# Optimization experiments

Hardware: AMD Instinct MI355X
Metric: run time of the kernel (lower is better)

## Reference

```python
import jax, jax.numpy as jnp
import numpy as np

B, LQ, LK, H = 4, 256, 512, 256

def setup_inputs() -> dict:
    key = jax.random.key(0)
    ks = jax.random.split(key, 9)
    return {
        "query": jax.random.normal(ks[0], (B, LQ, H), dtype=jnp.float32),
        "key": jax.random.normal(ks[1], (B, LK, H), dtype=jnp.float32),
        "value": jax.random.normal(ks[2], (B, LK, H), dtype=jnp.float32),
        "mask": jax.random.randint(ks[3], (B, LK), 0, 2, dtype=jnp.int32),
        "Wq": jax.random.normal(ks[4], (H, H), dtype=jnp.float32) / np.sqrt(H),
        "bq": jnp.zeros((H,), dtype=jnp.float32),
        "Wk": jax.random.normal(ks[5], (H, H), dtype=jnp.float32) / np.sqrt(H),
        "bk": jnp.zeros((H,), dtype=jnp.float32),
        "v": jax.random.normal(ks[6], (H,), dtype=jnp.float32) / np.sqrt(H),
        "bv": jnp.zeros((), dtype=jnp.float32),
    }

def reference(query, key, value, mask, Wq, bq, Wk, bk, v, bv):
    # Linear projections: y = x @ W^T + b (torch nn.Linear convention)
    q = query @ Wq.T + bq            # [B, Lq, H]
    k = key @ Wk.T + bk              # [B, Lk, H]
    # Broadcast add -> tanh -> project to scalar with v
    s = jnp.tanh(q[:, :, None, :] + k[:, None, :, :])   # [B, Lq, Lk, H]
    scores = jnp.einsum('bqkh,h->bqk', s, v) + bv        # [B, Lq, Lk]
    scores = jnp.where(mask[:, None, :] == 0, -jnp.inf, scores)
    attn_weights = jax.nn.softmax(scores, axis=-1)       # [B, Lq, Lk]
    attn_output = jnp.einsum('bqk,bkh->bqh', attn_weights, value)
    return (attn_output, attn_weights)
```

## Files before the change

kernel.cpp:

```cpp
#include <hip/hip_runtime.h>
#include <math.h>

#define NB  4
#define NLQ 256
#define NLK 512
#define NH  256

#define SCALE_2LOG2E 2.885390081777927f
#define LOG2E        1.4426950408889634f

__global__ __launch_bounds__(256) void setup_kernel(
    const float* __restrict__ Wq, const float* __restrict__ Wk,
    const int* __restrict__ mask,
    float* __restrict__ Wtq, float* __restrict__ Wtk,
    int* __restrict__ act, int* __restrict__ nact)
{
    const int blk = blockIdx.x;
    const int t   = threadIdx.x;

    if (blk < 32) {
        __shared__ float ts[64][65];
        const int m    = blk >> 4;
        const int tile = blk & 15;
        const int h0 = (tile >> 2) * 64;
        const int c0 = (tile & 3) * 64;
        const float* W  = m ? Wk  : Wq;
        float*       Wt = m ? Wtk : Wtq;
        const int lr = t >> 4, lc = t & 15;
        #pragma unroll
        for (int i = 0; i < 4; ++i) {
            const int r = lr + 16 * i;
            const float4 d = *(const float4*)(W + (size_t)(h0 + r) * NH + c0 + lc * 4);
            ts[r][lc * 4 + 0] = d.x;
            ts[r][lc * 4 + 1] = d.y;
            ts[r][lc * 4 + 2] = d.z;
            ts[r][lc * 4 + 3] = d.w;
        }
        __syncthreads();
        #pragma unroll
        for (int i = 0; i < 4; ++i) {
            const int c = lr + 16 * i;
            float4 d;
            d.x = ts[lc * 4 + 0][c];
            d.y = ts[lc * 4 + 1][c];
            d.z = ts[lc * 4 + 2][c];
            d.w = ts[lc * 4 + 3][c];
            *(float4*)(Wt + (size_t)(c0 + c) * NH + h0 + lc * 4) = d;
        }
    } else if (blk < 32 + NB) {
        const int b = blk - 32;
        __shared__ int wcnt[8], wpre[9];
        const int lane = t & 63, wave = t >> 6;
        const int k1 = t, k2 = t + 256;
        const int m1 = mask[b * NLK + k1];
        const int m2 = mask[b * NLK + k2];
        const unsigned long long below = (1ULL << lane) - 1ULL;
        const unsigned long long bal1 = __ballot(m1 != 0);
        const unsigned long long bal2 = __ballot(m2 != 0);
        const int r1 = __popcll(bal1 & below);
        const int r2 = __popcll(bal2 & below);
        if (lane == 0) { wcnt[wave] = __popcll(bal1); wcnt[4 + wave] = __popcll(bal2); }
        __syncthreads();
        if (t == 0) {
            int s = 0;
            #pragma unroll
            for (int w = 0; w < 8; ++w) { wpre[w] = s; s += wcnt[w]; }
            wpre[8] = s;
        }
        __syncthreads();
        const int na = wpre[8];
        if (m1) act[b * NLK + wpre[wave]     + r1] = k1;
        if (m2) act[b * NLK + wpre[4 + wave] + r2] = k2;
        if (k1 >= na) act[b * NLK + k1] = 0;
        if (k2 >= na) act[b * NLK + k2] = 0;
        if (t == 0) nact[b] = na;
    }
}

__global__ __launch_bounds__(256) void prep_kernel(
    const float* __restrict__ query, const float* __restrict__ key,
    const float* __restrict__ Wtq, const float* __restrict__ bq,
    const float* __restrict__ Wtk, const float* __restrict__ bk,
    const int* __restrict__ act, const int* __restrict__ nact,
    float* __restrict__ qp, float* __restrict__ kp_ct)
{
    const int blk  = blockIdx.x;
    const int t    = threadIdx.x;
    const int wave = t >> 6;
    const int lane = t & 63;

    __shared__ float  xs[4][NH];
    __shared__ float4 ps[4][4][64];
    __shared__ int    ridx[4];

    const float *Wt, *bias;
    int b = 0, j0 = 0, r0 = 0, na = 0;
    const bool isq = (blk < NB * NLQ / 4);

    if (isq) {
        r0 = blk * 4;
        ((float4*)&xs[0][0])[t] = ((const float4*)(query + (size_t)r0 * NH))[t];
        Wt = Wtq; bias = bq;
    } else {
        b  = (blk - 256) >> 7;
        j0 = ((blk - 256) & 127) * 4;
        na = nact[b];
        if (j0 >= na) return;
        if (t < 4) ridx[t] = act[b * NLK + ((j0 + t < na) ? (j0 + t) : j0)];
        __syncthreads();
        const int r = t >> 6, c4 = t & 63;
        ((float4*)xs[r])[c4] =
            ((const float4*)(key + ((size_t)b * NLK + ridx[r]) * NH))[c4];
        Wt = Wtk; bias = bk;
    }
    __syncthreads();

    float4 acc[4];
    #pragma unroll
    for (int r = 0; r < 4; ++r) acc[r] = (float4){0.f, 0.f, 0.f, 0.f};

    const int cbase = wave * 64;
    #pragma unroll 4
    for (int cc = 0; cc < 64; ++cc) {
        const int c = cbase + cc;
        const float4 w = *(const float4*)(Wt + (size_t)c * NH + lane * 4);
        #pragma unroll
        for (int r = 0; r < 4; ++r) {
            const float xv = xs[r][c];
            acc[r].x = fmaf(xv, w.x, acc[r].x);
            acc[r].y = fmaf(xv, w.y, acc[r].y);
            acc[r].z = fmaf(xv, w.z, acc[r].z);
            acc[r].w = fmaf(xv, w.w, acc[r].w);
        }
    }
    #pragma unroll
    for (int r = 0; r < 4; ++r) ps[wave][r][lane] = acc[r];
    __syncthreads();

    const int r = wave, l = lane;
    const float4 p0 = ps[0][r][l], p1 = ps[1][r][l];
    const float4 p2 = ps[2][r][l], p3 = ps[3][r][l];
    const float4 bb = *(const float4*)(bias + l * 4);
    float4 o;
    o.x = (p0.x + p1.x + p2.x + p3.x + bb.x) * SCALE_2LOG2E;
    o.y = (p0.y + p1.y + p2.y + p3.y + bb.y) * SCALE_2LOG2E;
    o.z = (p0.z + p1.z + p2.z + p3.z + bb.z) * SCALE_2LOG2E;
    o.w = (p0.w + p1.w + p2.w + p3.w + bb.w) * SCALE_2LOG2E;

    if (isq) {
        *(float4*)(qp + (size_t)(r0 + r) * NH + l * 4) = o;
    } else if (j0 + r < na) {
        const int j = j0 + r;
        kp_ct[((size_t)b * NH + l * 4 + 0) * NLK + j] = o.x;
        kp_ct[((size_t)b * NH + l * 4 + 1) * NLK + j] = o.y;
        kp_ct[((size_t)b * NH + l * 4 + 2) * NLK + j] = o.z;
        kp_ct[((size_t)b * NH + l * 4 + 3) * NLK + j] = o.w;
    }
}

__global__ __launch_bounds__(256) void attn_kernel(
    const float* __restrict__ qp, const float* __restrict__ kp_ct,
    const float* __restrict__ value, const int* __restrict__ mask,
    const int* __restrict__ act, const int* __restrict__ nact,
    const float* __restrict__ vvec,
    float* __restrict__ out_o, float* __restrict__ out_w)
{
    __shared__ float sc0[NLK], sc1[NLK];
    __shared__ int   actl[NLK];
    __shared__ float pA[256], pB[256], pC[256], pD[256];

    const int blk  = blockIdx.x;
    const int b    = blk >> 7;
    const int q0   = (blk & 127) * 2;
    const int t    = threadIdx.x;
    const int lane = t & 63;
    const int wave = t >> 6;

    const int na = nact[b];
    actl[t]       = (t < na)       ? act[b * NLK + t]       : 0;
    actl[t + 256] = (t + 256 < na) ? act[b * NLK + t + 256] : 0;

    float* w0row = out_w + (size_t)(b * NLQ + q0) * NLK;
    float* w1row = w0row + NLK;
    if (!mask[b * NLK + t])       { w0row[t] = 0.f;       w1row[t] = 0.f; }
    if (!mask[b * NLK + t + 256]) { w0row[t + 256] = 0.f; w1row[t + 256] = 0.f; }

    const int hh    = t >> 7;
    const int p     = t & 127;
    const int hbase = hh * 128;
    const float* qr0 = qp + (size_t)(b * NLQ + q0) * NH + hbase;
    const float* qr1 = qr0 + NH;
    const float* vvh = vvec + hbase;
    const float* kb  = kp_ct + ((size_t)b * NH + hbase) * NLK;

    float a00 = 0.f, a01 = 0.f, a10 = 0.f, a11 = 0.f;
    #pragma unroll 4
    for (int c = 0; c < 128; ++c) {
        const float2 kx = *(const float2*)(kb + (size_t)c * NLK + 2 * p);
        const float qa = qr0[c], qb = qr1[c], vh = vvh[c];
        const float e0 = __builtin_amdgcn_exp2f(qa + kx.x);
        const float e1 = __builtin_amdgcn_exp2f(qa + kx.y);
        const float e2 = __builtin_amdgcn_exp2f(qb + kx.x);
        const float e3 = __builtin_amdgcn_exp2f(qb + kx.y);
        a00 = fmaf(vh, __builtin_amdgcn_rcpf(e0 + 1.f), a00);
        a01 = fmaf(vh, __builtin_amdgcn_rcpf(e1 + 1.f), a01);
        a10 = fmaf(vh, __builtin_amdgcn_rcpf(e2 + 1.f), a10);
        a11 = fmaf(vh, __builtin_amdgcn_rcpf(e3 + 1.f), a11);
    }
    pA[t] = a00; pB[t] = a01; pC[t] = a10; pD[t] = a11;
    __syncthreads();
    if (t < 128) {
        const int s = 2 * t;
        sc0[s]     = (s     < na) ? -2.f * (pA[t] + pA[t + 128]) : -INFINITY;
        sc0[s + 1] = (s + 1 < na) ? -2.f * (pB[t] + pB[t + 128]) : -INFINITY;
    } else {
        const int p2 = t - 128;
        const int s  = 2 * p2;
        sc1[s]     = (s     < na) ? -2.f * (pC[p2] + pC[p2 + 128]) : -INFINITY;
        sc1[s + 1] = (s + 1 < na) ? -2.f * (pD[p2] + pD[p2 + 128]) : -INFINITY;
    }

    if (na > 256) {
        __syncthreads();
        a00 = a01 = a10 = a11 = 0.f;
        const int s0 = 256 + 2 * p;
        if (s0 < na) {
            #pragma unroll 4
            for (int c = 0; c < 128; ++c) {
                const float2 kx = *(const float2*)(kb + (size_t)c * NLK + s0);
                const float qa = qr0[c], qb = qr1[c], vh = vvh[c];
                const float e0 = __builtin_amdgcn_exp2f(qa + kx.x);
                const float e1 = __builtin_amdgcn_exp2f(qa + kx.y);
                const float e2 = __builtin_amdgcn_exp2f(qb + kx.x);
                const float e3 = __builtin_amdgcn_exp2f(qb + kx.y);
                a00 = fmaf(vh, __builtin_amdgcn_rcpf(e0 + 1.f), a00);
                a01 = fmaf(vh, __builtin_amdgcn_rcpf(e1 + 1.f), a01);
                a10 = fmaf(vh, __builtin_amdgcn_rcpf(e2 + 1.f), a10);
                a11 = fmaf(vh, __builtin_amdgcn_rcpf(e3 + 1.f), a11);
            }
        }
        pA[t] = a00; pB[t] = a01; pC[t] = a10; pD[t] = a11;
        __syncthreads();
        if (t < 128) {
            const int s = 256 + 2 * t;
            sc0[s]     = (s     < na) ? -2.f * (pA[t] + pA[t + 128]) : -INFINITY;
            sc0[s + 1] = (s + 1 < na) ? -2.f * (pB[t] + pB[t + 128]) : -INFINITY;
        } else {
            const int p2 = t - 128;
            const int s  = 256 + 2 * p2;
            sc1[s]     = (s     < na) ? -2.f * (pC[p2] + pC[p2 + 128]) : -INFINITY;
            sc1[s + 1] = (s + 1 < na) ? -2.f * (pD[p2] + pD[p2 + 128]) : -INFINITY;
        }
    } else {
        sc0[256 + t] = -INFINITY;
        sc1[256 + t] = -INFINITY;
    }
    __syncthreads();

    if (wave < 2) {
        float* row = wave ? sc1 : sc0;
        float vals[8];
        float m = -INFINITY;
        #pragma unroll
        for (int j8 = 0; j8 < 8; ++j8) {
            vals[j8] = row[lane + j8 * 64];
            m = fmaxf(m, vals[j8]);
        }
        #pragma unroll
        for (int s = 32; s >= 1; s >>= 1)
            m = fmaxf(m, __shfl_xor(m, s, 64));
        float sum = 0.0f;
        #pragma unroll
        for (int j8 = 0; j8 < 8; ++j8) {
            vals[j8] = __builtin_amdgcn_exp2f((vals[j8] - m) * LOG2E);
            sum += vals[j8];
        }
        #pragma unroll
        for (int s = 32; s >= 1; s >>= 1)
            sum += __shfl_xor(sum, s, 64);
        const float inv = __builtin_amdgcn_rcpf(sum);
        float* wout = out_w + (size_t)(b * NLQ + q0 + wave) * NLK;
        #pragma unroll
        for (int j8 = 0; j8 < 8; ++j8) {
            const int jj = lane + j8 * 64;
            const float w = vals[j8] * inv;
            row[jj] = w;
            if (jj < na) wout[actl[jj]] = w;
        }
    }
    __syncthreads();

    {
        const float* vb = value + (size_t)b * NLK * NH + t;
        float o0 = 0.f, o1 = 0.f;
        const int n4 = (na + 3) >> 2;
        for (int j4 = 0; j4 < n4; ++j4) {
            const float4 w0 = ((const float4*)sc0)[j4];
            const float4 w1 = ((const float4*)sc1)[j4];
            const int4   aj = ((const int4*)actl)[j4];
            const float v0 = vb[(size_t)aj.x * NH];
            const float v1 = vb[(size_t)aj.y * NH];
            const float v2 = vb[(size_t)aj.z * NH];
            const float v3 = vb[(size_t)aj.w * NH];
            o0 = fmaf(w0.x, v0, o0); o1 = fmaf(w1.x, v0, o1);
            o0 = fmaf(w0.y, v1, o0); o1 = fmaf(w1.y, v1, o1);
            o0 = fmaf(w0.z, v2, o0); o1 = fmaf(w1.z, v2, o1);
            o0 = fmaf(w0.w, v3, o0); o1 = fmaf(w1.w, v3, o1);
        }
        out_o[(size_t)(b * NLQ + q0)     * NH + t] = o0;
        out_o[(size_t)(b * NLQ + q0 + 1) * NH + t] = o1;
    }
}

extern "C" void kernel_launch(void* const* d_in, const int* in_sizes, int n_in,
                              void* d_out, int out_size, void* d_ws, size_t ws_size,
                              hipStream_t stream) {
    const float* query = (const float*)d_in[0];
    const float* key   = (const float*)d_in[1];
    const float* value = (const float*)d_in[2];
    const int*   mask  = (const int*)  d_in[3];
    const float* Wq    = (const float*)d_in[4];
    const float* bq    = (const float*)d_in[5];
    const float* Wk    = (const float*)d_in[6];
    const float* bk    = (const float*)d_in[7];
    const float* v     = (const float*)d_in[8];

    float* out_o = (float*)d_out;
    float* out_w = out_o + NB * NLQ * NH;

    float* qp    = (float*)d_ws;
    float* kp_ct = qp + NB * NLQ * NH;
    int*   act   = (int*)(kp_ct + NB * NH * NLK);
    int*   nact  = act + NB * NLK;

    const size_t base = (size_t)(NB * NLQ * NH) + (size_t)(NB * NH * NLK)
                      + NB * NLK + NB;
    float* wtq;
    if (ws_size >= (base + 2 * NH * NH) * sizeof(float)) {
        wtq = (float*)d_ws + base;
    } else {
        wtq = out_w + (size_t)NB * NLQ * NLK - 2 * NH * NH;
    }
    float* wtk = wtq + NH * NH;

    setup_kernel<<<36, 256, 0, stream>>>(Wq, Wk, mask, wtq, wtk, act, nact);
    prep_kernel<<<NB * NLQ / 4 + NB * NLK / 4, 256, 0, stream>>>(
        query, key, wtq, bq, wtk, bk, act, nact, qp, kp_ct);
    attn_kernel<<<NB * NLQ / 2, 256, 0, stream>>>(
        qp, kp_ct, value, mask, act, nact, v, out_o, out_w);
}
```

Before: 132.2 us.

## Precompute exp of projections so inner loop uses product instead of exp

```diff
diff --git a/kernel.cpp b/kernel.cpp
--- a/kernel.cpp
+++ b/kernel.cpp
@@ -146,6 +146,10 @@
     o.y = (p0.y + p1.y + p2.y + p3.y + bb.y) * SCALE_2LOG2E;
     o.z = (p0.z + p1.z + p2.z + p3.z + bb.z) * SCALE_2LOG2E;
     o.w = (p0.w + p1.w + p2.w + p3.w + bb.w) * SCALE_2LOG2E;
+    o.x = __builtin_amdgcn_exp2f(o.x);
+    o.y = __builtin_amdgcn_exp2f(o.y);
+    o.z = __builtin_amdgcn_exp2f(o.z);
+    o.w = __builtin_amdgcn_exp2f(o.w);
 
     if (isq) {
         *(float4*)(qp + (size_t)(r0 + r) * NH + l * 4) = o;
@@ -168,6 +172,9 @@
     __shared__ float sc0[NLK], sc1[NLK];
     __shared__ int   actl[NLK];
     __shared__ float pA[256], pB[256], pC[256], pD[256];
+    __shared__ float eqs[2][NH];
+    __shared__ float vvs[NH];
+    __shared__ float4 pr[2][256];
 
     const int blk  = blockIdx.x;
     const int b    = blk >> 7;
@@ -180,32 +187,32 @@
     actl[t]       = (t < na)       ? act[b * NLK + t]       : 0;
     actl[t + 256] = (t + 256 < na) ? act[b * NLK + t + 256] : 0;
 
+    eqs[0][t] = qp[(size_t)(b * NLQ + q0) * NH + t];
+    eqs[1][t] = qp[(size_t)(b * NLQ + q0 + 1) * NH + t];
+    vvs[t]    = vvec[t];
+
     float* w0row = out_w + (size_t)(b * NLQ + q0) * NLK;
     float* w1row = w0row + NLK;
     if (!mask[b * NLK + t])       { w0row[t] = 0.f;       w1row[t] = 0.f; }
     if (!mask[b * NLK + t + 256]) { w0row[t + 256] = 0.f; w1row[t + 256] = 0.f; }
-
-    const int hh    = t >> 7;
-    const int p     = t & 127;
-    const int hbase = hh * 128;
-    const float* qr0 = qp + (size_t)(b * NLQ + q0) * NH + hbase;
-    const float* qr1 = qr0 + NH;
-    const float* vvh = vvec + hbase;
-    const float* kb  = kp_ct + ((size_t)b * NH + hbase) * NLK;
+    __syncthreads();
+
+    const int hh = t >> 7;
+    const int p  = t & 127;
+    const int hb = hh * 128;
+    const float* kb = kp_ct + ((size_t)b * NH + hb) * NLK;
 
     float a00 = 0.f, a01 = 0.f, a10 = 0.f, a11 = 0.f;
     #pragma unroll 4
     for (int c = 0; c < 128; ++c) {
         const float2 kx = *(const float2*)(kb + (size_t)c * NLK + 2 * p);
-        const float qa = qr0[c], qb = qr1[c], vh = vvh[c];
-        const float e0 = __builtin_amdgcn_exp2f(qa + kx.x);
-        const float e1 = __builtin_amdgcn_exp2f(qa + kx.y);
-        const float e2 = __builtin_amdgcn_exp2f(qb + kx.x);
-        const float e3 = __builtin_amdgcn_exp2f(qb + kx.y);
-        a00 = fmaf(vh, __builtin_amdgcn_rcpf(e0 + 1.f), a00);
-        a01 = fmaf(vh, __builtin_amdgcn_rcpf(e1 + 1.f), a01);
-        a10 = fmaf(vh, __builtin_amdgcn_rcpf(e2 + 1.f), a10);
-        a11 = fmaf(vh, __builtin_amdgcn_rcpf(e3 + 1.f), a11);
+        const float eqa = eqs[0][hb + c];
+        const float eqb = eqs[1][hb + c];
+        const float vh  = vvs[hb + c];
+        a00 = fmaf(vh, __builtin_amdgcn_rcpf(fmaf(eqa, kx.x, 1.f)), a00);
+        a01 = fmaf(vh, __builtin_amdgcn_rcpf(fmaf(eqa, kx.y, 1.f)), a01);
+        a10 = fmaf(vh, __builtin_amdgcn_rcpf(fmaf(eqb, kx.x, 1.f)), a10);
+        a11 = fmaf(vh, __builtin_amdgcn_rcpf(fmaf(eqb, kx.y, 1.f)), a11);
     }
     pA[t] = a00; pB[t] = a01; pC[t] = a10; pD[t] = a11;
     __syncthreads();
@@ -228,15 +235,13 @@
             #pragma unroll 4
             for (int c = 0; c < 128; ++c) {
                 const float2 kx = *(const float2*)(kb + (size_t)c * NLK + s0);
-                const float qa = qr0[c], qb = qr1[c], vh = vvh[c];
-                const float e0 = __builtin_amdgcn_exp2f(qa + kx.x);
-                const float e1 = __builtin_amdgcn_exp2f(qa + kx.y);
-                const float e2 = __builtin_amdgcn_exp2f(qb + kx.x);
-                const float e3 = __builtin_amdgcn_exp2f(qb + kx.y);
-                a00 = fmaf(vh, __builtin_amdgcn_rcpf(e0 + 1.f), a00);
-                a01 = fmaf(vh, __builtin_amdgcn_rcpf(e1 + 1.f), a01);
-                a10 = fmaf(vh, __builtin_amdgcn_rcpf(e2 + 1.f), a10);
-                a11 = fmaf(vh, __builtin_amdgcn_rcpf(e3 + 1.f), a11);
+                const float eqa = eqs[0][hb + c];
+                const float eqb = eqs[1][hb + c];
+                const float vh  = vvs[hb + c];
+                a00 = fmaf(vh, __builtin_amdgcn_rcpf(fmaf(eqa, kx.x, 1.f)), a00);
+                a01 = fmaf(vh, __builtin_amdgcn_rcpf(fmaf(eqa, kx.y, 1.f)), a01);
+                a10 = fmaf(vh, __builtin_amdgcn_rcpf(fmaf(eqb, kx.x, 1.f)), a10);
+                a11 = fmaf(vh, __builtin_amdgcn_rcpf(fmaf(eqb, kx.y, 1.f)), a11);
             }
         }
         pA[t] = a00; pB[t] = a01; pC[t] = a10; pD[t] = a11;
@@ -291,24 +296,37 @@
     __syncthreads();
 
     {
-        const float* vb = value + (size_t)b * NLK * NH + t;
-        float o0 = 0.f, o1 = 0.f;
-        const int n4 = (na + 3) >> 2;
-        for (int j4 = 0; j4 < n4; ++j4) {
-            const float4 w0 = ((const float4*)sc0)[j4];
-            const float4 w1 = ((const float4*)sc1)[j4];
-            const int4   aj = ((const int4*)actl)[j4];
-            const float v0 = vb[(size_t)aj.x * NH];
-            const float v1 = vb[(size_t)aj.y * NH];
-            const float v2 = vb[(size_t)aj.z * NH];
-            const float v3 = vb[(size_t)aj.w * NH];
-            o0 = fmaf(w0.x, v0, o0); o1 = fmaf(w1.x, v0, o1);
-            o0 = fmaf(w0.y, v1, o0); o1 = fmaf(w1.y, v1, o1);
-            o0 = fmaf(w0.z, v2, o0); o1 = fmaf(w1.z, v2, o1);
-            o0 = fmaf(w0.w, v3, o0); o1 = fmaf(w1.w, v3, o1);
-        }
-        out_o[(size_t)(b * NLQ + q0)     * NH + t] = o0;
-        out_o[(size_t)(b * NLQ + q0 + 1) * NH + t] = o1;
+        const int c4 = lane * 4;
+        const float* vb = value + (size_t)b * NLK * NH + c4;
+        float4 o0 = {0.f, 0.f, 0.f, 0.f}, o1 = {0.f, 0.f, 0.f, 0.f};
+        #pragma unroll 4
+        for (int j = wave; j < na; j += 4) {
+            const float w0 = sc0[j];
+            const float w1 = sc1[j];
+            const int   rj = actl[j];
+            const float4 v4 = *(const float4*)(vb + (size_t)rj * NH);
+            o0.x = fmaf(w0, v4.x, o0.x); o0.y = fmaf(w0, v4.y, o0.y);
+            o0.z = fmaf(w0, v4.z, o0.z); o0.w = fmaf(w0, v4.w, o0.w);
+            o1.x = fmaf(w1, v4.x, o1.x); o1.y = fmaf(w1, v4.y, o1.y);
+            o1.z = fmaf(w1, v4.z, o1.z); o1.w = fmaf(w1, v4.w, o1.w);
+        }
+        pr[0][t] = o0;
+        pr[1][t] = o1;
+        __syncthreads();
+        if (t < 128) {
+            const int row = t >> 6;
+            const int l   = t & 63;
+            const float4 s0 = pr[row][l];
+            const float4 s1 = pr[row][l + 64];
+            const float4 s2 = pr[row][l + 128];
+            const float4 s3 = pr[row][l + 192];
+            float4 o;
+            o.x = s0.x + s1.x + s2.x + s3.x;
+            o.y = s0.y + s1.y + s2.y + s3.y;
+            o.z = s0.z + s1.z + s2.z + s3.z;
+            o.w = s0.w + s1.w + s2.w + s3.w;
+            *(float4*)(out_o + (size_t)(b * NLQ + q0 + row) * NH + l * 4) = o;
+        }
     }
 }
 
```

After: 120.8 us. 8.6% less time.
